# Kernel optimization log

Hardware: AMD Instinct MI355X
Metric: run time of the kernel (lower is better)

## Reference

```python
import jax, jax.numpy as jnp
import numpy as np

HEADS = 12
HEAD_SIZE = 64
NEG = 1e12


def _rope_tables(seq_len, head_size, dtype=jnp.float32):
    pos = jnp.arange(seq_len, dtype=dtype)[:, None]                      # [s,1]
    idx = jnp.arange(0, head_size, 2, dtype=dtype)                       # [hs/2]
    ang = pos / (10000.0 ** (idx / head_size))                           # [s,hs/2]
    sin = jnp.repeat(jnp.sin(ang), 2, axis=-1)                           # [s,hs]
    cos = jnp.repeat(jnp.cos(ang), 2, axis=-1)                           # [s,hs]
    return sin[None, :, None, :], cos[None, :, None, :]                  # [1,s,1,hs]


def _rotate_half_interleaved(x):
    # pairs (x0,x1) -> (-x1, x0), interleaved layout
    x2 = jnp.stack([-x[..., 1::2], x[..., ::2]], axis=-1)
    return x2.reshape(x.shape)


def setup_inputs() -> dict:
    key = jax.random.key(0)
    k1, k2, k3 = jax.random.split(key, 3)
    b, s, d = 8, 1024, 1024
    inputs = jax.random.normal(k1, (b, s, d), dtype=jnp.float32)
    W = jax.random.normal(k2, (d, HEADS * HEAD_SIZE * 2), dtype=jnp.float32) * 0.02
    bias = jnp.zeros((HEADS * HEAD_SIZE * 2,), dtype=jnp.float32)
    lengths = jax.random.randint(k3, (b,), s // 2, s + 1)
    mask = (jnp.arange(s)[None, :] < lengths[:, None]).astype(jnp.int32)  # [b,s]
    return {"inputs": inputs, "W": W, "bias": bias, "mask": mask}


def reference(inputs, W, bias, mask):
    b, s, _ = inputs.shape
    proj = inputs @ W + bias                                             # [b,s,2*h*hs]
    proj = proj.reshape(b, s, HEADS, 2 * HEAD_SIZE)
    qw, kw = proj[..., :HEAD_SIZE], proj[..., HEAD_SIZE:]
    sin, cos = _rope_tables(s, HEAD_SIZE, dtype=qw.dtype)
    qw = qw * cos + _rotate_half_interleaved(qw) * sin
    kw = kw * cos + _rotate_half_interleaved(kw) * sin
    logits = jnp.einsum('bmhd,bnhd->bhmn', qw, kw)                       # [b,h,m,n]
    m = mask.astype(logits.dtype)
    logits = logits - (1.0 - m)[:, None, None, :] * NEG                  # key padding
    logits = logits - (1.0 - m)[:, None, :, None] * NEG                  # query padding
    tri = (jnp.arange(s)[:, None] > jnp.arange(s)[None, :]).astype(logits.dtype)
    logits = logits - tri * NEG                                          # lower-tri (diag=-1)
    return logits / (HEAD_SIZE ** 0.5)
```

## Files before the change

kernel.cpp:

```cpp
#include <hip/hip_runtime.h>
#include <hip/hip_bf16.h>
#include <stdint.h>

#define NHEADS 12
#define HSZ 64
#define BATCH 8
#define SEQ 1024
#define DIN 1024
#define NPROJ 1536
#define MTOK 8192
#define NEGV 1e12f

typedef float  f32x4  __attribute__((ext_vector_type(4)));
typedef __bf16 bf16x8 __attribute__((ext_vector_type(8)));

__device__ __forceinline__ ushort f2bf(float x) {
  union { float f; uint32_t u; } v; v.f = x;
  uint32_t r = v.u + 0x7FFFu + ((v.u >> 16) & 1u);
  return (ushort)(r >> 16);
}

__device__ __forceinline__ void async16(const void* g, void* l) {
  __builtin_amdgcn_global_load_lds(
      (const __attribute__((address_space(1))) uint32_t*)g,
      (__attribute__((address_space(3))) uint32_t*)l,
      16, 0, 0);
}

__global__ __launch_bounds__(256) void k_prep(
    const float* __restrict__ inp, const float* __restrict__ W,
    ushort* __restrict__ A16, ushort* __restrict__ Wt, float* __restrict__ tab) {
  const int blk = blockIdx.x;
  const int tid = threadIdx.x;
  if (blk < 2048) {
    const float4* in4 = (const float4*)inp;
    ushort4* out4 = (ushort4*)A16;
    const int n4 = MTOK * DIN / 4;
    int i = blk * 256 + tid;
    for (; i < n4; i += 2048 * 256) {
      float4 v = in4[i];
      ushort4 o;
      o.x = f2bf(v.x); o.y = f2bf(v.y); o.z = f2bf(v.z); o.w = f2bf(v.w);
      out4[i] = o;
    }
  } else if (blk < 2432) {
    __shared__ float tile[64][65];
    const int bb = blk - 2048;
    const int n0 = (bb % 24) * 64;
    const int k0 = (bb / 24) * 64;
    const int c  = tid & 63;
    const int r0 = (tid >> 6) * 16;
    #pragma unroll
    for (int rr = 0; rr < 16; ++rr)
      tile[r0 + rr][c] = W[(size_t)(k0 + r0 + rr) * NPROJ + n0 + c];
    __syncthreads();
    #pragma unroll
    for (int rr = 0; rr < 16; ++rr)
      Wt[(size_t)(n0 + r0 + rr) * DIN + k0 + c] = f2bf(tile[c][r0 + rr]);
  } else {
    const int t = (blk - 2432) * 256 + tid;
    const int s = t >> 5, i = t & 31;
    const float p   = powf(10000.0f, (float)i / 32.0f);
    const float ang = (float)s / p;
    tab[2 * t]     = sinf(ang);
    tab[2 * t + 1] = cosf(ang);
  }
}

__global__ __launch_bounds__(256, 3) void k_gemm_proj(
    const ushort* __restrict__ A, const ushort* __restrict__ Bt,
    const float* __restrict__ bias, const float* __restrict__ tab,
    ushort* __restrict__ Qb, ushort* __restrict__ Kb) {
  __shared__ __align__(16) ushort As[3][128 * 32];
  __shared__ __align__(16) ushort Bs[3][128 * 32];
  const int tid  = threadIdx.x;
  const int lane = tid & 63;
  const int wid  = tid >> 6;
  const int wm = wid >> 1, wn = wid & 1;
  const int orig = blockIdx.x;
  const int wgid = (orig & 7) * 96 + (orig >> 3);
  const int m0 = (wgid / 12) * 128;
  const int n0 = (wgid % 12) * 128;

  const int off0 = tid * 16;
  const int off1 = 4096 + tid * 16;
  const int r0 = off0 >> 6, s0 = (off0 >> 4) & 3;
  const int r1 = off1 >> 6, s1 = (off1 >> 4) & 3;
  const int g0 = (s0 ^ ((r0 >> 1) & 3)) * 8;
  const int g1 = (s1 ^ ((r1 >> 1) & 3)) * 8;
  const ushort* gA0 = A  + (size_t)(m0 + r0) * DIN + g0;
  const ushort* gA1 = A  + (size_t)(m0 + r1) * DIN + g1;
  const ushort* gB0 = Bt + (size_t)(n0 + r0) * DIN + g0;
  const ushort* gB1 = Bt + (size_t)(n0 + r1) * DIN + g1;

  const int kb = lane >> 4;
  int aoff[4], boff[4];
  #pragma unroll
  for (int i = 0; i < 4; ++i) {
    const int ra = wm * 64 + i * 16 + (lane & 15);
    aoff[i] = ra * 32 + (kb ^ ((ra >> 1) & 3)) * 8;
    const int rb = wn * 64 + i * 16 + (lane & 15);
    boff[i] = rb * 32 + (kb ^ ((rb >> 1) & 3)) * 8;
  }

  const int lA = wid * 512;
  const int lB = 2048 + wid * 512;

  ushort *a0 = As[0], *a1 = As[1], *a2 = As[2];
  ushort *b0 = Bs[0], *b1 = Bs[1], *b2 = Bs[2];

  f32x4 acc[4][4] = {};
  async16(gA0,      a0 + lA); async16(gA1,      a0 + lB);
  async16(gB0,      b0 + lA); async16(gB1,      b0 + lB);
  async16(gA0 + 32, a1 + lA); async16(gA1 + 32, a1 + lB);
  async16(gB0 + 32, b1 + lA); async16(gB1 + 32, b1 + lB);

  for (int kt = 0; kt < 31; ++kt) {
    asm volatile("s_waitcnt vmcnt(4)" ::: "memory");
    __builtin_amdgcn_s_barrier();
    if (kt < 30) {
      const int ko = (kt + 2) * 32;
      async16(gA0 + ko, a2 + lA); async16(gA1 + ko, a2 + lB);
      async16(gB0 + ko, b2 + lA); async16(gB1 + ko, b2 + lB);
    }
    bf16x8 af[4], bfr[4];
    #pragma unroll
    for (int i = 0; i < 4; ++i) {
      af[i]  = *(const bf16x8*)(a0 + aoff[i]);
      bfr[i] = *(const bf16x8*)(b0 + boff[i]);
    }
    #pragma unroll
    for (int mi = 0; mi < 4; ++mi)
      #pragma unroll
      for (int ni = 0; ni < 4; ++ni)
        acc[mi][ni] = __builtin_amdgcn_mfma_f32_16x16x32_bf16(af[mi], bfr[ni], acc[mi][ni], 0, 0, 0);
    ushort* ta = a0; a0 = a1; a1 = a2; a2 = ta;
    ushort* tb = b0; b0 = b1; b1 = b2; b2 = tb;
  }
  asm volatile("s_waitcnt vmcnt(0)" ::: "memory");
  __builtin_amdgcn_s_barrier();
  {
    bf16x8 af[4], bfr[4];
    #pragma unroll
    for (int i = 0; i < 4; ++i) {
      af[i]  = *(const bf16x8*)(a0 + aoff[i]);
      bfr[i] = *(const bf16x8*)(b0 + boff[i]);
    }
    #pragma unroll
    for (int mi = 0; mi < 4; ++mi)
      #pragma unroll
      for (int ni = 0; ni < 4; ++ni)
        acc[mi][ni] = __builtin_amdgcn_mfma_f32_16x16x32_bf16(af[mi], bfr[ni], acc[mi][ni], 0, 0, 0);
  }

  const int b = m0 >> 10;
  const int baserow = m0 + wm * 64 + ((lane >> 4) << 2);
  #pragma unroll
  for (int ni = 0; ni < 4; ++ni) {
    const int n = n0 + wn * 64 + ni * 16 + (lane & 15);
    const float bv = bias[n];
    const int h  = n >> 7;
    const int c  = n & 127;
    const int d  = c & 63;
    const int pi = d >> 1;
    ushort* dst = ((c < 64) ? Qb : Kb) + (size_t)(b * NHEADS + h) * SEQ * 64 + d;
    #pragma unroll
    for (int mi = 0; mi < 4; ++mi) {
      #pragma unroll
      for (int j = 0; j < 4; ++j) {
        const int gm = baserow + mi * 16 + j;
        const int s  = gm & (SEQ - 1);
        float v = acc[mi][ni][j] + bv;
        float p = __shfl_xor(v, 1);
        float2 sc = ((const float2*)tab)[s * 32 + pi];
        float o = (d & 1) ? fmaf(v, sc.y, p * sc.x) : fmaf(v, sc.y, -p * sc.x);
        dst[(size_t)s * 64] = f2bf(o);
      }
    }
  }
}

__global__ __launch_bounds__(256) void k_out(
    const ushort* __restrict__ Qb, const ushort* __restrict__ Kb,
    const int* __restrict__ mask, float* __restrict__ out) {
  __shared__ __align__(16) ushort Qs[128 * 64];
  __shared__ __align__(16) ushort Ks[128 * 64];
  const int tid  = threadIdx.x;
  const int orig = blockIdx.x;
  const int wgid = (orig & 7) * 768 + (orig >> 3);
  const int bh = wgid >> 6;
  const int b  = bh / NHEADS;
  const int mi_ = (wgid >> 3) & 7;
  const int ni_ = wgid & 7;
  const int m0 = mi_ * 128;
  const int n0 = ni_ * 128;
  const int* mb = mask + b * SEQ;
  float* ob = out + (size_t)bh * SEQ * SEQ;

  if (mi_ > ni_) {
    const int c0 = (tid & 31) * 4;
    const int r0 = tid >> 5;
    f32x4 np4;
    #pragma unroll
    for (int j = 0; j < 4; ++j) np4[j] = mb[n0 + c0 + j] ? 0.0f : NEGV;
    for (int r = r0; r < 128; r += 8) {
      const int gm = m0 + r;
      const float mp = (mb[gm] ? 0.0f : NEGV) + NEGV;
      f32x4 v;
      #pragma unroll
      for (int j = 0; j < 4; ++j) v[j] = -(np4[j] + mp) * 0.125f;
      __builtin_nontemporal_store(v, (f32x4*)(ob + (size_t)gm * SEQ + n0 + c0));
    }
    return;
  }

  const int lane = tid & 63;
  const int wid  = tid >> 6;
  const int wm = wid >> 1, wn = wid & 1;
  const ushort* Qt = Qb + (size_t)bh * SEQ * 64;
  const ushort* Kt = Kb + (size_t)bh * SEQ * 64;

  #pragma unroll
  for (int is = 0; is < 4; ++is) {
    const int off = is * 4096 + tid * 16;
    const int row = off >> 7;
    const int g8  = ((((off >> 4) & 7) ^ (row & 7))) * 8;
    async16(Qt + (size_t)(m0 + row) * 64 + g8, Qs + is * 2048 + wid * 512);
    async16(Kt + (size_t)(n0 + row) * 64 + g8, Ks + is * 2048 + wid * 512);
  }
  __syncthreads();

  f32x4 acc[4][4] = {};
  const int kb = lane >> 4;
  #pragma unroll
  for (int ks = 0; ks < 2; ++ks) {
    bf16x8 qf[4], kf[4];
    #pragma unroll
    for (int i = 0; i < 4; ++i) {
      const int rq = wm * 64 + i * 16 + (lane & 15);
      qf[i] = *(const bf16x8*)(Qs + rq * 64 + ((ks * 4 + kb) ^ (rq & 7)) * 8);
      const int rk = wn * 64 + i * 16 + (lane & 15);
      kf[i] = *(const bf16x8*)(Ks + rk * 64 + ((ks * 4 + kb) ^ (rk & 7)) * 8);
    }
    #pragma unroll
    for (int mi = 0; mi < 4; ++mi)
      #pragma unroll
      for (int ni = 0; ni < 4; ++ni)
        acc[mi][ni] = __builtin_amdgcn_mfma_f32_16x16x32_bf16(qf[mi], kf[ni], acc[mi][ni], 0, 0, 0);
  }

  const int mrow0 = m0 + wm * 64 + ((lane >> 4) << 2);
  const int ncol0 = n0 + wn * 64 + (lane & 15);
  float npen[4];
  int gn_[4];
  #pragma unroll
  for (int ni = 0; ni < 4; ++ni) {
    gn_[ni]  = ncol0 + ni * 16;
    npen[ni] = mb[gn_[ni]] ? 0.0f : NEGV;
  }
  #pragma unroll
  for (int mi = 0; mi < 4; ++mi) {
    #pragma unroll
    for (int j = 0; j < 4; ++j) {
      const int gm = mrow0 + mi * 16 + j;
      const float mpen = mb[gm] ? 0.0f : NEGV;
      float* orow = ob + (size_t)gm * SEQ;
      #pragma unroll
      for (int ni = 0; ni < 4; ++ni) {
        const int gn = gn_[ni];
        const float tpen = (gm > gn) ? NEGV : 0.0f;
        orow[gn] = (acc[mi][ni][j] - (mpen + npen[ni] + tpen)) * 0.125f;
      }
    }
  }
}

extern "C" void kernel_launch(void* const* d_in, const int* in_sizes, int n_in,
                              void* d_out, int out_size, void* d_ws, size_t ws_size,
                              hipStream_t stream) {
  const float* inp  = (const float*)d_in[0];
  const float* W    = (const float*)d_in[1];
  const float* bias = (const float*)d_in[2];
  const int*   mask = (const int*)d_in[3];
  float* out = (float*)d_out;

  char* ws = (char*)d_ws;
  ushort* A16  = (ushort*)ws;
  ushort* WT16 = (ushort*)(ws + 16777216);
  float*  tab  = (float*)(ws + 19922944);
  ushort* Qb   = (ushort*)(ws + 20185088);
  ushort* Kb   = (ushort*)(ws + 32768000);

  k_prep<<<2560, 256, 0, stream>>>(inp, W, A16, WT16, tab);
  k_gemm_proj<<<768, 256, 0, stream>>>(A16, WT16, bias, tab, Qb, Kb);
  k_out<<<6144, 256, 0, stream>>>(Qb, Kb, mask, out);
}
```

Baseline: 118.2 us.

## Widen projection GEMM tile to 128x384 with 512-thread blocks

The projection GEMM now uses 128x384 output tiles computed by 8 waves (each 64x96) instead of 128x128 tiles with 4 waves. It launches 256 workgroups, one per CU, with a remapped tile-to-block order. The larger N tile lets each A tile load be reused across three times as many columns, cutting global and LDS traffic per FLOP. The cost is more LDS per block (about 96KB) and more accumulator registers, which likely limits a CU to one resident block and so reduces latency hiding.

```diff
diff --git a/kernel.cpp b/kernel.cpp
--- a/kernel.cpp
+++ b/kernel.cpp
@@ -67,72 +67,80 @@
   }
 }
 
-__global__ __launch_bounds__(256, 3) void k_gemm_proj(
+__global__ __launch_bounds__(512, 2) void k_gemm_proj(
     const ushort* __restrict__ A, const ushort* __restrict__ Bt,
     const float* __restrict__ bias, const float* __restrict__ tab,
     ushort* __restrict__ Qb, ushort* __restrict__ Kb) {
   __shared__ __align__(16) ushort As[3][128 * 32];
-  __shared__ __align__(16) ushort Bs[3][128 * 32];
+  __shared__ __align__(16) ushort Bs[3][384 * 32];
   const int tid  = threadIdx.x;
   const int lane = tid & 63;
   const int wid  = tid >> 6;
-  const int wm = wid >> 1, wn = wid & 1;
-  const int orig = blockIdx.x;
-  const int wgid = (orig & 7) * 96 + (orig >> 3);
-  const int m0 = (wgid / 12) * 128;
-  const int n0 = (wgid % 12) * 128;
-
-  const int off0 = tid * 16;
-  const int off1 = 4096 + tid * 16;
-  const int r0 = off0 >> 6, s0 = (off0 >> 4) & 3;
-  const int r1 = off1 >> 6, s1 = (off1 >> 4) & 3;
-  const int g0 = (s0 ^ ((r0 >> 1) & 3)) * 8;
-  const int g1 = (s1 ^ ((r1 >> 1) & 3)) * 8;
-  const ushort* gA0 = A  + (size_t)(m0 + r0) * DIN + g0;
-  const ushort* gA1 = A  + (size_t)(m0 + r1) * DIN + g1;
-  const ushort* gB0 = Bt + (size_t)(n0 + r0) * DIN + g0;
-  const ushort* gB1 = Bt + (size_t)(n0 + r1) * DIN + g1;
+  const int wm = wid >> 2, wn = wid & 3;
+  const int orig  = blockIdx.x;
+  const int local = orig >> 3;
+  const int mt = (orig & 7) * 8 + (local >> 2);
+  const int nt = local & 3;
+  const int m0 = mt * 128;
+  const int n0 = nt * 384;
+
+  const int rA  = tid >> 2;
+  const int sl  = tid & 3;
+  const int gA8 = (sl ^ ((rA >> 1) & 3)) * 8;
+  const ushort* gA = A + (size_t)(m0 + rA) * DIN + gA8;
+  const ushort* gB[3];
+  #pragma unroll
+  for (int is = 0; is < 3; ++is) {
+    const int rB = rA + is * 128;
+    const int gB8 = (sl ^ ((rB >> 1) & 3)) * 8;
+    gB[is] = Bt + (size_t)(n0 + rB) * DIN + gB8;
+  }
+  const int ldsA = wid * 512;
+  int ldsB[3];
+  #pragma unroll
+  for (int is = 0; is < 3; ++is) ldsB[is] = is * 4096 + wid * 512;
 
   const int kb = lane >> 4;
-  int aoff[4], boff[4];
+  int aoff[4], boff[6];
   #pragma unroll
   for (int i = 0; i < 4; ++i) {
     const int ra = wm * 64 + i * 16 + (lane & 15);
     aoff[i] = ra * 32 + (kb ^ ((ra >> 1) & 3)) * 8;
-    const int rb = wn * 64 + i * 16 + (lane & 15);
+  }
+  #pragma unroll
+  for (int i = 0; i < 6; ++i) {
+    const int rb = wn * 96 + i * 16 + (lane & 15);
     boff[i] = rb * 32 + (kb ^ ((rb >> 1) & 3)) * 8;
   }
-
-  const int lA = wid * 512;
-  const int lB = 2048 + wid * 512;
 
   ushort *a0 = As[0], *a1 = As[1], *a2 = As[2];
   ushort *b0 = Bs[0], *b1 = Bs[1], *b2 = Bs[2];
 
-  f32x4 acc[4][4] = {};
-  async16(gA0,      a0 + lA); async16(gA1,      a0 + lB);
-  async16(gB0,      b0 + lA); async16(gB1,      b0 + lB);
-  async16(gA0 + 32, a1 + lA); async16(gA1 + 32, a1 + lB);
-  async16(gB0 + 32, b1 + lA); async16(gB1 + 32, b1 + lB);
+  f32x4 acc[4][6] = {};
+  async16(gA, a0 + ldsA);
+  async16(gB[0], b0 + ldsB[0]); async16(gB[1], b0 + ldsB[1]); async16(gB[2], b0 + ldsB[2]);
+  async16(gA + 32, a1 + ldsA);
+  async16(gB[0] + 32, b1 + ldsB[0]); async16(gB[1] + 32, b1 + ldsB[1]); async16(gB[2] + 32, b1 + ldsB[2]);
 
   for (int kt = 0; kt < 31; ++kt) {
     asm volatile("s_waitcnt vmcnt(4)" ::: "memory");
     __builtin_amdgcn_s_barrier();
     if (kt < 30) {
       const int ko = (kt + 2) * 32;
-      async16(gA0 + ko, a2 + lA); async16(gA1 + ko, a2 + lB);
-      async16(gB0 + ko, b2 + lA); async16(gB1 + ko, b2 + lB);
-    }
-    bf16x8 af[4], bfr[4];
-    #pragma unroll
-    for (int i = 0; i < 4; ++i) {
-      af[i]  = *(const bf16x8*)(a0 + aoff[i]);
-      bfr[i] = *(const bf16x8*)(b0 + boff[i]);
-    }
+      async16(gA + ko, a2 + ldsA);
+      async16(gB[0] + ko, b2 + ldsB[0]);
+      async16(gB[1] + ko, b2 + ldsB[1]);
+      async16(gB[2] + ko, b2 + ldsB[2]);
+    }
+    bf16x8 af[4], bfr[6];
+    #pragma unroll
+    for (int i = 0; i < 4; ++i) af[i]  = *(const bf16x8*)(a0 + aoff[i]);
+    #pragma unroll
+    for (int i = 0; i < 6; ++i) bfr[i] = *(const bf16x8*)(b0 + boff[i]);
     #pragma unroll
     for (int mi = 0; mi < 4; ++mi)
       #pragma unroll
-      for (int ni = 0; ni < 4; ++ni)
+      for (int ni = 0; ni < 6; ++ni)
         acc[mi][ni] = __builtin_amdgcn_mfma_f32_16x16x32_bf16(af[mi], bfr[ni], acc[mi][ni], 0, 0, 0);
     ushort* ta = a0; a0 = a1; a1 = a2; a2 = ta;
     ushort* tb = b0; b0 = b1; b1 = b2; b2 = tb;
@@ -140,24 +148,23 @@
   asm volatile("s_waitcnt vmcnt(0)" ::: "memory");
   __builtin_amdgcn_s_barrier();
   {
-    bf16x8 af[4], bfr[4];
-    #pragma unroll
-    for (int i = 0; i < 4; ++i) {
-      af[i]  = *(const bf16x8*)(a0 + aoff[i]);
-      bfr[i] = *(const bf16x8*)(b0 + boff[i]);
-    }
+    bf16x8 af[4], bfr[6];
+    #pragma unroll
+    for (int i = 0; i < 4; ++i) af[i]  = *(const bf16x8*)(a0 + aoff[i]);
+    #pragma unroll
+    for (int i = 0; i < 6; ++i) bfr[i] = *(const bf16x8*)(b0 + boff[i]);
     #pragma unroll
     for (int mi = 0; mi < 4; ++mi)
       #pragma unroll
-      for (int ni = 0; ni < 4; ++ni)
+      for (int ni = 0; ni < 6; ++ni)
         acc[mi][ni] = __builtin_amdgcn_mfma_f32_16x16x32_bf16(af[mi], bfr[ni], acc[mi][ni], 0, 0, 0);
   }
 
   const int b = m0 >> 10;
   const int baserow = m0 + wm * 64 + ((lane >> 4) << 2);
   #pragma unroll
-  for (int ni = 0; ni < 4; ++ni) {
-    const int n = n0 + wn * 64 + ni * 16 + (lane & 15);
+  for (int ni = 0; ni < 6; ++ni) {
+    const int n = n0 + wn * 96 + ni * 16 + (lane & 15);
     const float bv = bias[n];
     const int h  = n >> 7;
     const int c  = n & 127;
@@ -292,6 +299,6 @@
   ushort* Kb   = (ushort*)(ws + 32768000);
 
   k_prep<<<2560, 256, 0, stream>>>(inp, W, A16, WT16, tab);
-  k_gemm_proj<<<768, 256, 0, stream>>>(A16, WT16, bias, tab, Qb, Kb);
+  k_gemm_proj<<<256, 512, 0, stream>>>(A16, WT16, bias, tab, Qb, Kb);
   k_out<<<6144, 256, 0, stream>>>(Qb, Kb, mask, out);
 }
```

New measurement: 118.2 us. No clear change (+0.0%).
